# Optimization experiments

Hardware: AMD Instinct MI355X
Metric: run time of the kernel (lower is better)

The kernel has to match this reference:

```python
import jax
import jax.numpy as jnp
import numpy as np

NPOINT = 512
RADIUS = 0.2
K = 32


def setup_inputs() -> dict:
    key = jax.random.key(0)
    k1, k2 = jax.random.split(key)
    xyz = jax.random.uniform(k1, (8, 16384, 3), dtype=jnp.float32)      # [B,N,3] in unit cube
    features = jax.random.normal(k2, (8, 128, 16384), dtype=jnp.float32)  # [B,D,N]
    return {"xyz": xyz, "features": features}


def farthest_point_sample(xyz, npoint):
    # xyz: [B,N,3] -> centroids [B,npoint] int32. Deterministic start at index 0
    # (the torch code does randint(...)*0).
    B, N, _ = xyz.shape
    init_dist = jnp.full((B, N), 1e10, dtype=xyz.dtype)
    init_far = jnp.zeros((B,), dtype=jnp.int32)

    def step(carry, _):
        distance, farthest = carry
        centroid = jnp.take_along_axis(xyz, farthest[:, None, None], axis=1)  # [B,1,3]
        d = jnp.sum((xyz - centroid) ** 2, axis=-1)                           # [B,N]
        distance = jnp.minimum(distance, d)
        new_far = jnp.argmax(distance, axis=-1).astype(jnp.int32)
        return (distance, new_far), farthest

    (_, _), cents = jax.lax.scan(step, (init_dist, init_far), None, length=npoint)
    return cents.T  # [B, npoint]


def square_distance(src, dst):
    # src [B,S,3], dst [B,N,3] -> [B,S,N]
    d = -2.0 * jnp.einsum("bsc,bnc->bsn", src, dst)
    d = d + jnp.sum(src ** 2, -1)[:, :, None]
    d = d + jnp.sum(dst ** 2, -1)[:, None, :]
    return d


def query_ball_point(radius, nsample, xyz, new_xyz):
    B, N, _ = xyz.shape
    sqrd = square_distance(new_xyz, xyz)                              # [B,S,N]
    arangeN = jnp.arange(N, dtype=jnp.int32)[None, None, :]
    idx = jnp.where(sqrd > radius ** 2, N, arangeN)                   # out-of-ball -> sentinel N
    idx = jnp.sort(idx, axis=-1)[:, :, :nsample]                      # [B,S,K]
    first = idx[:, :, :1]
    idx = jnp.where(idx == N, first, idx)                             # pad with first valid neighbor
    return idx


def index_points(points, idx):
    # points [B,N,C], idx [B,...] -> [B,...,C]
    B = points.shape[0]
    bidx = jnp.arange(B).reshape((B,) + (1,) * (idx.ndim - 1))
    return points[bidx, idx]


def reference(xyz, features):
    # xyz [B,N,3], features [B,D,N]
    cent = farthest_point_sample(xyz, NPOINT)                 # [B,S]
    new_xyz = index_points(xyz, cent)                         # [B,S,3]
    idx = query_ball_point(RADIUS, K, xyz, new_xyz)           # [B,S,K]
    pts = jnp.transpose(features, (0, 2, 1))                  # [B,N,D]
    grouped = index_points(pts, idx)                          # [B,S,K,D]
    sub_features = jnp.max(grouped, axis=2)                   # [B,S,D]  (max over K neighbors)
    sub_features = jnp.transpose(sub_features, (0, 2, 1))     # [B,D,S]
    return new_xyz, sub_features
```

## Files before the change

### kernel.cpp

```cpp
#include <hip/hip_runtime.h>
#include <stdint.h>
#include <math.h>

#define NB      8
#define NPTS    16384
#define NPOINT  512
#define NCH     128
#define KNBR    32
#define R2      0.04f

#define FPS_THR 512
#define PPT     (NPTS / FPS_THR)

#define CENT_OFF 0
#define FT_OFF   16384

#define DPP_ARG_STEP(v, p, CTRL) do {                                          \
    float _ov = __builtin_bit_cast(float, __builtin_amdgcn_update_dpp(         \
        __builtin_bit_cast(int, (v)), __builtin_bit_cast(int, (v)),            \
        (CTRL), 0xF, 0xF, false));                                             \
    int _op = __builtin_amdgcn_update_dpp((p), (p), (CTRL), 0xF, 0xF, false);  \
    bool _t = (_ov > (v)) || ((_ov == (v)) && (_op < (p)));                    \
    (v) = _t ? _ov : (v);                                                      \
    (p) = _t ? _op : (p);                                                      \
} while (0)

#define SHFL_ARG_STEP(v, p, XORAMT) do {                                       \
    float _ov = __shfl_xor((v), (XORAMT), 64);                                 \
    int   _op = __shfl_xor((p), (XORAMT), 64);                                 \
    bool _t = (_ov > (v)) || ((_ov == (v)) && (_op < (p)));                    \
    (v) = _t ? _ov : (v);                                                      \
    (p) = _t ? _op : (p);                                                      \
} while (0)

__global__
__attribute__((amdgpu_flat_work_group_size(FPS_THR, FPS_THR)))
__attribute__((amdgpu_waves_per_eu(2, 4)))
void fps_transpose_kernel(const float* __restrict__ xyz,
                          const float* __restrict__ feat,
                          float* __restrict__ out,
                          int* __restrict__ cent,
                          float* __restrict__ ft,
                          int use_ft)
{
    const int blk = blockIdx.x;
    const int tid = threadIdx.x;

    if (blk < NB) {
        const int b = blk;
        const float* xb = xyz + (size_t)b * NPTS * 3;
        float px[PPT], py[PPT], pz[PPT], d[PPT];
#pragma unroll
        for (int k = 0; k < PPT; ++k) {
            int p = k * FPS_THR + tid;
            px[k] = xb[p * 3 + 0];
            py[k] = xb[p * 3 + 1];
            pz[k] = xb[p * 3 + 2];
            d[k] = 1e10f;
        }
        __shared__ float s_v[2][32];
        __shared__ int   s_p[2][32];
        const int lane = tid & 63;
        const int wid  = tid >> 6;

        float cx = xb[0], cy = xb[1], cz = xb[2];
        if (tid == 0) {
            cent[b * NPOINT + 0] = 0;
            out[((size_t)b * NPOINT + 0) * 3 + 0] = cx;
            out[((size_t)b * NPOINT + 0) * 3 + 1] = cy;
            out[((size_t)b * NPOINT + 0) * 3 + 2] = cz;
        }

        for (int i = 1; i < NPOINT; ++i) {
            float vmax = -1.0f;
#pragma unroll
            for (int k = 0; k < PPT; ++k) {
                float dx = __fsub_rn(px[k], cx);
                float dy = __fsub_rn(py[k], cy);
                float dz = __fsub_rn(pz[k], cz);
                float dd = __fadd_rn(__fadd_rn(__fmul_rn(dx, dx),
                                               __fmul_rn(dy, dy)),
                                     __fmul_rn(dz, dz));
                float nd = fminf(d[k], dd);
                d[k] = nd;
                vmax = fmaxf(vmax, nd);
            }
            int bk = PPT - 1;
#pragma unroll
            for (int k = PPT - 2; k >= 0; --k) bk = (d[k] == vmax) ? k : bk;

            float rv = vmax;
            int   rp = bk * FPS_THR + tid;
            DPP_ARG_STEP(rv, rp, 0xB1);
            DPP_ARG_STEP(rv, rp, 0x4E);
            DPP_ARG_STEP(rv, rp, 0x141);
            DPP_ARG_STEP(rv, rp, 0x140);
            const int par = i & 1;
            if ((lane & 15) == 0) {
                int slot = wid * 4 + (lane >> 4);
                s_v[par][slot] = rv;
                s_p[par][slot] = rp;
            }
            __syncthreads();
            float fv = s_v[par][lane & 31];
            int   fp = s_p[par][lane & 31];
            DPP_ARG_STEP(fv, fp, 0xB1);
            DPP_ARG_STEP(fv, fp, 0x4E);
            DPP_ARG_STEP(fv, fp, 0x141);
            DPP_ARG_STEP(fv, fp, 0x140);
            SHFL_ARG_STEP(fv, fp, 16);
            const int cur = __builtin_amdgcn_readfirstlane(fp);
            cx = xb[cur * 3 + 0];
            cy = xb[cur * 3 + 1];
            cz = xb[cur * 3 + 2];
            if (tid == 0) {
                cent[b * NPOINT + i] = cur;
                size_t o = ((size_t)b * NPOINT + i) * 3;
                out[o + 0] = cx; out[o + 1] = cy; out[o + 2] = cz;
            }
        }
    } else {
        if (!use_ft) return;
        int t  = blk - NB;
        int b  = t >> 11;
        int r  = t & 2047;
        int ct = r >> 9;
        int nt = r & 511;
        __shared__ float tile[32][33];
        int tx = tid & 31, ty = tid >> 5;
        tile[ty][tx] =
            feat[((size_t)b * NCH + ct * 32 + ty) * NPTS + nt * 32 + tx];
        tile[ty + 16][tx] =
            feat[((size_t)b * NCH + ct * 32 + ty + 16) * NPTS + nt * 32 + tx];
        __syncthreads();
        ft[((size_t)b * NPTS + nt * 32 + ty) * NCH + ct * 32 + tx] =
            tile[tx][ty];
        ft[((size_t)b * NPTS + nt * 32 + ty + 16) * NCH + ct * 32 + tx] =
            tile[tx][ty + 16];
    }
}

__global__ __launch_bounds__(256, 4)
void query_pool_kernel(const float* __restrict__ xyz,
                       const float* __restrict__ feat,
                       const float* __restrict__ ft,
                       const int* __restrict__ cent,
                       float* __restrict__ out_sub,
                       int use_ft)
{
    const int tid  = threadIdx.x;
    const int widx = tid >> 6;
    const int lane = tid & 63;
    const int w = blockIdx.x * 4 + widx;
    const int b = w >> 9;
    const int s = w & 511;

    const float* xb = xyz + (size_t)b * NPTS * 3;
    const int ci = cent[b * NPOINT + s];
    const float sx = xb[ci * 3 + 0];
    const float sy = xb[ci * 3 + 1];
    const float sz = xb[ci * 3 + 2];
    const float snorm = __fadd_rn(__fadd_rn(__fmul_rn(sx, sx),
                                            __fmul_rn(sy, sy)),
                                  __fmul_rn(sz, sz));

    __shared__ int lidx[4][KNBR];
    int found = 0;
    for (int base = 0; base < NPTS && found < KNBR; base += 64) {
        int j = base + lane;
        float dx = xb[j * 3 + 0];
        float dy = xb[j * 3 + 1];
        float dz = xb[j * 3 + 2];
        float dn = __fadd_rn(__fadd_rn(__fmul_rn(dx, dx),
                                       __fmul_rn(dy, dy)),
                             __fmul_rn(dz, dz));
        float dot = __fadd_rn(__fadd_rn(__fmul_rn(sx, dx),
                                        __fmul_rn(sy, dy)),
                              __fmul_rn(sz, dz));
        float d = __fadd_rn(__fadd_rn(__fmul_rn(-2.0f, dot), snorm), dn);
        bool inball = !(d > R2);
        unsigned long long mask = __ballot(inball);
        int before = (int)__popcll(mask & ((1ULL << lane) - 1ULL));
        int slot = found + before;
        if (inball && slot < KNBR) lidx[widx][slot] = j;
        found += (int)__popcll(mask);
    }
    int cnt = found < KNBR ? found : KNBR;
    __syncthreads();

    float a0 = -INFINITY, a1 = -INFINITY;
    if (use_ft) {
        for (int m = 0; m < cnt; ++m) {
            int i = lidx[widx][m];
            const float* row = ft + ((size_t)b * NPTS + i) * NCH;
            a0 = fmaxf(a0, row[lane]);
            a1 = fmaxf(a1, row[lane + 64]);
        }
    } else {
        for (int m = 0; m < cnt; ++m) {
            int i = lidx[widx][m];
            a0 = fmaxf(a0, feat[((size_t)b * NCH + lane) * NPTS + i]);
            a1 = fmaxf(a1, feat[((size_t)b * NCH + lane + 64) * NPTS + i]);
        }
    }
    out_sub[((size_t)b * NCH + lane) * NPOINT + s] = a0;
    out_sub[((size_t)b * NCH + lane + 64) * NPOINT + s] = a1;
}

extern "C" void kernel_launch(void* const* d_in, const int* in_sizes, int n_in,
                              void* d_out, int out_size, void* d_ws, size_t ws_size,
                              hipStream_t stream)
{
    const float* xyz  = (const float*)d_in[0];
    const float* feat = (const float*)d_in[1];
    float* out = (float*)d_out;

    int*   cent = (int*)((char*)d_ws + CENT_OFF);
    float* ft   = (float*)((char*)d_ws + FT_OFF);
    const size_t need_ft = FT_OFF + (size_t)NB * NPTS * NCH * 4ull;
    int use_ft = (ws_size >= need_ft) ? 1 : 0;

    int nblocks1 = NB + (use_ft ? NB * (NCH / 32) * (NPTS / 32) : 0);
    hipLaunchKernelGGL(fps_transpose_kernel, dim3(nblocks1), dim3(FPS_THR), 0, stream,
                       xyz, feat, out, cent, ft, use_ft);

    hipLaunchKernelGGL(query_pool_kernel, dim3((NB * NPOINT) / 4), dim3(256), 0, stream,
                       xyz, feat, ft, cent, out + (size_t)NB * NPOINT * 3, use_ft);
}
```

Before: 1.107 ms.

## Morton-sort FPS points into spatial buckets and skip far buckets via bounds

Before the farthest-point-sampling loop, each batch's points are bucketed into an 8x8x8 Morton-ordered grid with a shared-memory histogram and prefix scan, and the point indices are scattered to a workspace map. Each lane's group of 64 points then gets a bounding sphere. Per iteration, a group is skipped when its sphere is provably farther from the new centroid than an upper bound on its current min-distances. This removes most distance updates in later iterations, at the cost of setup work, a sqrt per group per iteration, branch divergence, and extra register pressure from storing original indices.

```diff
diff --git a/kernel.cpp b/kernel.cpp
--- a/kernel.cpp
+++ b/kernel.cpp
@@ -10,10 +10,11 @@
 #define R2      0.04f
 
 #define FPS_THR 512
-#define PPT     (NPTS / FPS_THR)
+#define PPT     32
 
 #define CENT_OFF 0
-#define FT_OFF   16384
+#define MAP_OFF  16384
+#define FT_OFF   (16384 + 524288)
 
 #define DPP_ARG_STEP(v, p, CTRL) do {                                          \
     float _ov = __builtin_bit_cast(float, __builtin_amdgcn_update_dpp(         \
@@ -33,13 +34,25 @@
     (p) = _t ? _op : (p);                                                      \
 } while (0)
 
+__device__ __forceinline__ int cell_of(float x, float y, float z) {
+    int cx = (int)(x * 8.0f); cx = cx < 0 ? 0 : (cx > 7 ? 7 : cx);
+    int cy = (int)(y * 8.0f); cy = cy < 0 ? 0 : (cy > 7 ? 7 : cy);
+    int cz = (int)(z * 8.0f); cz = cz < 0 ? 0 : (cz > 7 ? 7 : cz);
+    int m = 0;
+    m |= ((cx & 1) << 2) | ((cx & 2) << 4) | ((cx & 4) << 6);
+    m |= ((cy & 1) << 1) | ((cy & 2) << 3) | ((cy & 4) << 5);
+    m |=  (cz & 1)       | ((cz & 2) << 2) | ((cz & 4) << 4);
+    return m;
+}
+
 __global__
 __attribute__((amdgpu_flat_work_group_size(FPS_THR, FPS_THR)))
-__attribute__((amdgpu_waves_per_eu(2, 4)))
+__attribute__((amdgpu_waves_per_eu(2, 2)))
 void fps_transpose_kernel(const float* __restrict__ xyz,
                           const float* __restrict__ feat,
                           float* __restrict__ out,
                           int* __restrict__ cent,
+                          int* __restrict__ map,
                           float* __restrict__ ft,
                           int use_ft)
 {
@@ -49,19 +62,85 @@
     if (blk < NB) {
         const int b = blk;
         const float* xb = xyz + (size_t)b * NPTS * 3;
-        float px[PPT], py[PPT], pz[PPT], d[PPT];
-#pragma unroll
+        int* gmap = map + b * NPTS;
+        const int lane = tid & 63;
+        const int wid  = tid >> 6;
+
+        __shared__ int   s_hist[512];
+        __shared__ float s_meta[8][32][4];
+        __shared__ float s_v[2][32];
+        __shared__ int   s_p[2][32];
+
+        s_hist[tid] = 0;
+        __syncthreads();
         for (int k = 0; k < PPT; ++k) {
             int p = k * FPS_THR + tid;
-            px[k] = xb[p * 3 + 0];
-            py[k] = xb[p * 3 + 1];
-            pz[k] = xb[p * 3 + 2];
-            d[k] = 1e10f;
-        }
-        __shared__ float s_v[2][32];
-        __shared__ int   s_p[2][32];
-        const int lane = tid & 63;
-        const int wid  = tid >> 6;
+            int c = cell_of(xb[p * 3 + 0], xb[p * 3 + 1], xb[p * 3 + 2]);
+            atomicAdd(&s_hist[c], 1);
+        }
+        __syncthreads();
+        int mycount = s_hist[tid];
+        for (int off = 1; off < 512; off <<= 1) {
+            int v = (tid >= off) ? s_hist[tid - off] : 0;
+            __syncthreads();
+            s_hist[tid] += v;
+            __syncthreads();
+        }
+        int excl = s_hist[tid] - mycount;
+        __syncthreads();
+        s_hist[tid] = excl;
+        __syncthreads();
+        for (int k = 0; k < PPT; ++k) {
+            int p = k * FPS_THR + tid;
+            int c = cell_of(xb[p * 3 + 0], xb[p * 3 + 1], xb[p * 3 + 2]);
+            int pos = atomicAdd(&s_hist[c], 1);
+            gmap[pos] = p;
+        }
+        __threadfence_block();
+        __syncthreads();
+        float px[PPT], py[PPT], pz[PPT], d[PPT];
+        int   idx[PPT];
+#pragma unroll
+        for (int k = 0; k < PPT; ++k) {
+            int pos = wid * 2048 + k * 64 + lane;
+            int op  = gmap[pos];
+            idx[k] = op;
+            px[k] = xb[op * 3 + 0];
+            py[k] = xb[op * 3 + 1];
+            pz[k] = xb[op * 3 + 2];
+            d[k]  = 1e10f;
+        }
+#pragma unroll
+        for (int k = 0; k < PPT; ++k) {
+            float mnx = px[k], mxx = px[k];
+            float mny = py[k], mxy = py[k];
+            float mnz = pz[k], mxz = pz[k];
+#pragma unroll
+            for (int s = 1; s < 64; s <<= 1) {
+                mnx = fminf(mnx, __shfl_xor(mnx, s, 64));
+                mxx = fmaxf(mxx, __shfl_xor(mxx, s, 64));
+                mny = fminf(mny, __shfl_xor(mny, s, 64));
+                mxy = fmaxf(mxy, __shfl_xor(mxy, s, 64));
+                mnz = fminf(mnz, __shfl_xor(mnz, s, 64));
+                mxz = fmaxf(mxz, __shfl_xor(mxz, s, 64));
+            }
+            if (lane == 0) {
+                float hx = (mxx - mnx) * 0.5f;
+                float hy = (mxy - mny) * 0.5f;
+                float hz = (mxz - mnz) * 0.5f;
+                s_meta[wid][k][0] = (mnx + mxx) * 0.5f;
+                s_meta[wid][k][1] = (mny + mxy) * 0.5f;
+                s_meta[wid][k][2] = (mnz + mxz) * 0.5f;
+                s_meta[wid][k][3] =
+                    sqrtf(hx * hx + hy * hy + hz * hz) * 1.0001f + 1e-6f;
+            }
+        }
+        __syncthreads();
+        const float bmx = s_meta[wid][lane & 31][0];
+        const float bmy = s_meta[wid][lane & 31][1];
+        const float bmz = s_meta[wid][lane & 31][2];
+        const float br  = s_meta[wid][lane & 31][3];
+        float U = 1e10f;
 
         float cx = xb[0], cy = xb[1], cz = xb[2];
         if (tid == 0) {
@@ -72,25 +151,39 @@
         }
 
         for (int i = 1; i < NPOINT; ++i) {
-            float vmax = -1.0f;
-#pragma unroll
-            for (int k = 0; k < PPT; ++k) {
-                float dx = __fsub_rn(px[k], cx);
-                float dy = __fsub_rn(py[k], cy);
-                float dz = __fsub_rn(pz[k], cz);
-                float dd = __fadd_rn(__fadd_rn(__fmul_rn(dx, dx),
-                                               __fmul_rn(dy, dy)),
-                                     __fmul_rn(dz, dz));
-                float nd = fminf(d[k], dd);
-                d[k] = nd;
-                vmax = fmaxf(vmax, nd);
-            }
-            int bk = PPT - 1;
-#pragma unroll
-            for (int k = PPT - 2; k >= 0; --k) bk = (d[k] == vmax) ? k : bk;
+            float dcx = cx - bmx, dcy = cy - bmy, dcz = cz - bmz;
+            float dc  = sqrtf(dcx * dcx + dcy * dcy + dcz * dcz);
+            float t   = dc - br;
+            bool skip = (t > 0.0f) && (t * t >= U + 2e-5f);
+            unsigned mask = (unsigned)__ballot(skip);
+
+            if (mask != 0xFFFFFFFFu) {
+#pragma unroll
+                for (int k = 0; k < PPT; ++k) {
+                    if (!(mask & (1u << k))) {
+                        float dx = __fsub_rn(px[k], cx);
+                        float dy = __fsub_rn(py[k], cy);
+                        float dz = __fsub_rn(pz[k], cz);
+                        float dd = __fadd_rn(__fadd_rn(__fmul_rn(dx, dx),
+                                                       __fmul_rn(dy, dy)),
+                                             __fmul_rn(dz, dz));
+                        d[k] = fminf(d[k], dd);
+                    }
+                }
+            }
+            if (!((mask >> (lane & 31)) & 1u)) {
+                float ub = dc + br;
+                U = fminf(U, ub * ub * 1.0001f + 1e-6f);
+            }
+            float vmax = d[0];
+#pragma unroll
+            for (int k = 1; k < PPT; ++k) vmax = fmaxf(vmax, d[k]);
+            int bi = idx[PPT - 1];
+#pragma unroll
+            for (int k = PPT - 2; k >= 0; --k) bi = (d[k] == vmax) ? idx[k] : bi;
 
             float rv = vmax;
-            int   rp = bk * FPS_THR + tid;
+            int   rp = bi;
             DPP_ARG_STEP(rv, rp, 0xB1);
             DPP_ARG_STEP(rv, rp, 0x4E);
             DPP_ARG_STEP(rv, rp, 0x141);
@@ -216,13 +309,14 @@
     float* out = (float*)d_out;
 
     int*   cent = (int*)((char*)d_ws + CENT_OFF);
+    int*   map  = (int*)((char*)d_ws + MAP_OFF);
     float* ft   = (float*)((char*)d_ws + FT_OFF);
-    const size_t need_ft = FT_OFF + (size_t)NB * NPTS * NCH * 4ull;
+    const size_t need_ft = (size_t)FT_OFF + (size_t)NB * NPTS * NCH * 4ull;
     int use_ft = (ws_size >= need_ft) ? 1 : 0;
 
     int nblocks1 = NB + (use_ft ? NB * (NCH / 32) * (NPTS / 32) : 0);
     hipLaunchKernelGGL(fps_transpose_kernel, dim3(nblocks1), dim3(FPS_THR), 0, stream,
-                       xyz, feat, out, cent, ft, use_ft);
+                       xyz, feat, out, cent, map, ft, use_ft);
 
     hipLaunchKernelGGL(query_pool_kernel, dim3((NB * NPOINT) / 4), dim3(256), 0, stream,
                        xyz, feat, ft, cent, out + (size_t)NB * NPOINT * 3, use_ft);
```

Result: faster. 1.081 ms (-2.3%).
